# Kernel optimization log

Measured on AMD Instinct MI355X. Metric: run time of the kernel, lower is better.

The kernel has to match this reference:

```python
import jax, jax.numpy as jnp
import numpy as np
from jax import lax

N, C, RC, H, W = 2, 256, 32, 64, 64  # RC = C // 8


def conv1x1(x, w, b):
    # x: [n,c,h,w], w: [o,c], b: [o]
    return jnp.einsum('nchw,oc->nohw', x, w) + b[None, :, None, None]


def conv3x3(x, w, b):
    # x: [n,c,h,w], w: [o,i,3,3]
    y = lax.conv_general_dilated(x, w, window_strides=(1, 1), padding='SAME',
                                 dimension_numbers=('NCHW', 'OIHW', 'NCHW'))
    return y + b[None, :, None, None]


def setup_inputs() -> dict:
    key = jax.random.key(0)
    ks = jax.random.split(key, 16)
    p = lambda k, s: jax.random.normal(k, s, dtype=jnp.float32) * 0.02
    z = lambda o: jnp.zeros((o,), jnp.float32)
    return {
        'rgb_feat': jax.random.normal(ks[0], (N, C, H, W), jnp.float32),
        'chm_feat': jax.random.normal(ks[1], (N, C, H, W), jnp.float32),
        'rgb_q_w': p(ks[2], (RC, C)), 'rgb_q_b': z(RC),
        'rgb_k_w': p(ks[3], (RC, C)), 'rgb_k_b': z(RC),
        'rgb_v_w': p(ks[4], (C, C)), 'rgb_v_b': z(C),
        'depth_q_w': p(ks[5], (RC, C)), 'depth_q_b': z(RC),
        'depth_k_w': p(ks[6], (RC, C)), 'depth_k_b': z(RC),
        'depth_v_w': p(ks[7], (C, C)), 'depth_v_b': z(C),
        'gate_w': p(ks[8], (C, 2 * C)), 'gate_b': z(C),
        'fus1_w': p(ks[9], (2 * C, 2 * C)), 'fus1_b': z(2 * C),
        'fus2_w': p(ks[10], (2 * C, 2 * C, 3, 3)), 'fus2_b': z(2 * C),
        'fus3_w': p(ks[11], (C, 2 * C)), 'fus3_b': z(C),
        'skip_w': p(ks[12], (C, 2 * C)), 'skip_b': z(C),
    }


def reference(rgb_feat, chm_feat,
              rgb_q_w, rgb_q_b, rgb_k_w, rgb_k_b, rgb_v_w, rgb_v_b,
              depth_q_w, depth_q_b, depth_k_w, depth_k_b, depth_v_w, depth_v_b,
              gate_w, gate_b, fus1_w, fus1_b, fus2_w, fus2_b,
              fus3_w, fus3_b, skip_w, skip_b):
    n, c, h, w = rgb_feat.shape
    hw = h * w
    flat = lambda t: t.reshape(n, t.shape[1], hw)

    rq = flat(conv1x1(rgb_feat, rgb_q_w, rgb_q_b))       # [n,rc,hw]
    rk = flat(conv1x1(rgb_feat, rgb_k_w, rgb_k_b))       # [n,rc,hw]
    rv = flat(conv1x1(rgb_feat, rgb_v_w, rgb_v_b))       # [n,c,hw]
    dq = flat(conv1x1(chm_feat, depth_q_w, depth_q_b))   # [n,rc,hw]
    dk = flat(conv1x1(chm_feat, depth_k_w, depth_k_b))   # [n,rc,hw]
    dv = flat(conv1x1(chm_feat, depth_v_w, depth_v_b))   # [n,c,hw]

    # rgb branch attended with depth-derived attention
    rgb_attn = jax.nn.softmax(jnp.einsum('nri,nrj->nij', dq, dk), axis=-1)  # [n,hw,hw]
    br = jnp.einsum('nci,nij->ncj', rv, rgb_attn).reshape(rgb_feat.shape) + rgb_feat

    # depth branch attended with rgb-derived attention
    depth_attn = jax.nn.softmax(jnp.einsum('nri,nrj->nij', rq, rk), axis=-1)
    bd = jnp.einsum('nci,nij->ncj', dv, depth_attn).reshape(chm_feat.shape) + chm_feat

    cat = jnp.concatenate([br, bd], axis=1)              # [n,2c,h,w]
    g = jax.nn.sigmoid(conv1x1(cat, gate_w, gate_b))     # [n,c,h,w]
    c_fused = br * g + bd * (1.0 - g)
    d_fused = br * bd
    f = jnp.concatenate([c_fused, d_fused], axis=1)      # [n,2c,h,w]

    y = jax.nn.relu(conv1x1(f, fus1_w, fus1_b))
    y = jax.nn.relu(conv3x3(y, fus2_w, fus2_b))
    y = conv1x1(y, fus3_w, fus3_b)
    fused = y + conv1x1(f, skip_w, skip_b)
    return fused
```

## Files before the change

kernel.cpp:

```cpp
#include <hip/hip_runtime.h>
#include <stdint.h>


typedef __bf16 bf16_t;
typedef __bf16 bf16x8 __attribute__((ext_vector_type(8)));
typedef float f32x4 __attribute__((ext_vector_type(4)));

#define HW 4096
#define NB 2

__device__ inline f32x4 mfma_bf16(bf16x8 a, bf16x8 b, f32x4 c) {
    return __builtin_amdgcn_mfma_f32_16x16x32_bf16(a, b, c, 0, 0, 0);
}

#define LBAR()                                                                 \
    do {                                                                       \
        asm volatile("s_waitcnt lgkmcnt(0)" ::: "memory");                     \
        __builtin_amdgcn_s_barrier();                                          \
        __builtin_amdgcn_sched_barrier(0);                                     \
    } while (0)

#define MAXJOB 12
struct CvtJobs {
    const float* src[MAXJOB];
    bf16_t* dst[MAXJOB];
    int vend[MAXJOB];
    int rowlen[MAXJOB];
    int rowstride[MAXJOB];
    int rowoff[MAXJOB];
};

__global__ __launch_bounds__(256) void prep_k(CvtJobs J, int totalvec, int cvtBlocks,
                                              const float* __restrict__ fus2_src,
                                              bf16_t* __restrict__ fus2_dst,
                                              const float* qr, const float* kr,
                                              const float* qd, const float* kd,
                                              const float* sb, const float* fb,
                                              float* BQK_R, float* BQK_D, float* BSUM) {
    const int b = blockIdx.x, t = threadIdx.x;
    if (b < cvtBlocks) {
        int gv = b * 256 + t;
        if (gv >= totalvec) return;
        int j = 0;
        while (gv >= J.vend[j]) j++;
        int vbase = (j == 0) ? 0 : J.vend[j - 1];
        int e = (gv - vbase) * 8;
        const float* s = J.src[j] + e;
        float4 f0 = *(const float4*)s;
        float4 f1 = *(const float4*)(s + 4);
        bf16x8 o;
        o[0] = (bf16_t)f0.x; o[1] = (bf16_t)f0.y; o[2] = (bf16_t)f0.z; o[3] = (bf16_t)f0.w;
        o[4] = (bf16_t)f1.x; o[5] = (bf16_t)f1.y; o[6] = (bf16_t)f1.z; o[7] = (bf16_t)f1.w;
        int di = e;
        if (J.rowlen[j])
            di = (e / J.rowlen[j]) * J.rowstride[j] + J.rowoff[j] + (e % J.rowlen[j]);
        *(bf16x8*)(J.dst[j] + di) = o;
    } else if (b < cvtBlocks + 9216) {
        int idx = (b - cvtBlocks) * 256 + t;
        int o = idx / 4608;
        int tt = idx % 4608;
        int t9 = tt / 512;
        int c  = tt % 512;
        fus2_dst[idx] = (bf16_t)fus2_src[(size_t)o * 4608 + c * 9 + t9];
    } else {
        if (t < 32) {
            BQK_R[t] = qr[t]; BQK_R[32 + t] = kr[t];
            BQK_D[t] = qd[t]; BQK_D[32 + t] = kd[t];
        }
        BSUM[t] = sb[t] + fb[t];
    }
}

__global__ __launch_bounds__(512) void proj_k(const bf16_t* __restrict__ WV_R,
                                              const bf16_t* __restrict__ WV_D,
                                              const bf16_t* __restrict__ WQK_R,
                                              const bf16_t* __restrict__ WQK_D,
                                              const bf16_t* __restrict__ XB,
                                              const float* __restrict__ vb_r,
                                              const float* __restrict__ vb_d,
                                              const float* __restrict__ bqk_r,
                                              const float* __restrict__ bqk_d,
                                              bf16_t* __restrict__ V4,
                                              bf16_t* __restrict__ QKT) {
    __shared__ bf16_t Bt[2][64][72];
    const int t = threadIdx.x, b = blockIdx.x;
    const int w = t >> 6, lane = t & 63, quad = lane >> 4, l16 = lane & 15;

    f32x4 zero = {0.f, 0.f, 0.f, 0.f};
    f32x4 acc[4] = {zero, zero, zero, zero};

    if (b < 512) {
        const int mb = b & 1, jb = (b >> 1) & 63, n = b >> 7;
        const bf16_t* Au = (n >= 2) ? WV_D : WV_R;
        const float* biasu = (n >= 2) ? vb_d : vb_r;
        const bf16_t* Bb = XB + (size_t)n * (256 * HW) + jb * 64;
        const bf16_t* Arow = Au + (size_t)(mb * 128 + w * 16 + l16) * 256 + quad * 8;

        bf16x8 v0 = *(const bf16x8*)(Bb + (size_t)lane * HW + w * 8);
        for (int k0 = 0; k0 < 256; k0 += 64) {
            LBAR();
#pragma unroll
            for (int e = 0; e < 8; e++) Bt[0][w * 8 + e][lane] = v0[e];
            LBAR();
            const int kn = (k0 + 64 < 256) ? k0 + 64 : 0;
            bf16x8 vp = *(const bf16x8*)(Bb + (size_t)(kn + lane) * HW + w * 8);
            bf16x8 a0 = *(const bf16x8*)(Arow + k0);
            bf16x8 a1 = *(const bf16x8*)(Arow + k0 + 32);
#pragma unroll
            for (int ns = 0; ns < 4; ns++) {
                bf16x8 b0 = *(const bf16x8*)&Bt[0][ns * 16 + l16][quad * 8];
                bf16x8 b1 = *(const bf16x8*)&Bt[0][ns * 16 + l16][32 + quad * 8];
                acc[ns] = mfma_bf16(a0, b0, acc[ns]);
                acc[ns] = mfma_bf16(a1, b1, acc[ns]);
            }
            v0 = vp;
        }
#pragma unroll
        for (int ns = 0; ns < 4; ns++) {
#pragma unroll
            for (int rr = 0; rr < 4; rr++) {
                int m = mb * 128 + w * 16 + quad * 4 + rr;
                int col = jb * 64 + ns * 16 + l16;
                V4[(size_t)n * 256 * HW + (size_t)m * HW + col] =
                    (bf16_t)(acc[ns][rr] + biasu[m]);
            }
        }
    } else {
        const int qb = b - 512;
        const int n2 = qb >> 5, jpair = qb & 31;
        const int g = w >> 2, wg = w & 3;
        const int jb = jpair * 2 + g;
        const bf16_t* Au = (n2 >= 2) ? WQK_D : WQK_R;
        const float* biasu = (n2 >= 2) ? bqk_d : bqk_r;
        const bf16_t* Bb = XB + (size_t)n2 * (256 * HW) + jb * 64;
        const bf16_t* Arow = Au + (size_t)(wg * 16 + l16) * 256 + quad * 8;

        bf16x8 v0 = *(const bf16x8*)(Bb + (size_t)lane * HW + wg * 16);
        bf16x8 v1 = *(const bf16x8*)(Bb + (size_t)lane * HW + wg * 16 + 8);
        for (int k0 = 0; k0 < 256; k0 += 64) {
            LBAR();
#pragma unroll
            for (int e = 0; e < 8; e++) Bt[g][wg * 16 + e][lane] = v0[e];
#pragma unroll
            for (int e = 0; e < 8; e++) Bt[g][wg * 16 + 8 + e][lane] = v1[e];
            LBAR();
            const int kn = (k0 + 64 < 256) ? k0 + 64 : 0;
            bf16x8 p0 = *(const bf16x8*)(Bb + (size_t)(kn + lane) * HW + wg * 16);
            bf16x8 p1 = *(const bf16x8*)(Bb + (size_t)(kn + lane) * HW + wg * 16 + 8);
            bf16x8 a0 = *(const bf16x8*)(Arow + k0);
            bf16x8 a1 = *(const bf16x8*)(Arow + k0 + 32);
#pragma unroll
            for (int ns = 0; ns < 4; ns++) {
                bf16x8 b0 = *(const bf16x8*)&Bt[g][ns * 16 + l16][quad * 8];
                bf16x8 b1 = *(const bf16x8*)&Bt[g][ns * 16 + l16][32 + quad * 8];
                acc[ns] = mfma_bf16(a0, b0, acc[ns]);
                acc[ns] = mfma_bf16(a1, b1, acc[ns]);
            }
            v0 = p0; v1 = p1;
        }
        const float scl = (wg < 2) ? 1.44269504f : 1.0f;
#pragma unroll
        for (int ns = 0; ns < 4; ns++) {
            int col = jb * 64 + ns * 16 + l16;
            union { bf16_t h[4]; unsigned long long u; } pk;
#pragma unroll
            for (int rr = 0; rr < 4; rr++) {
                int m = wg * 16 + quad * 4 + rr;
                pk.h[rr] = (bf16_t)((acc[ns][rr] + biasu[m]) * scl);
            }
            *(unsigned long long*)(QKT +
                ((size_t)n2 * HW + col) * 64 + wg * 16 + quad * 4) = pk.u;
        }
    }
}

template <int EPI, bool OUT_BF16>
__global__ __launch_bounds__(512) void gemm_k(const bf16_t* __restrict__ A,
                                              const bf16_t* __restrict__ A2,
                                              const bf16_t* __restrict__ B,
                                              const float* __restrict__ bias,
                                              const float* __restrict__ bias2,
                                              void* __restrict__ outp,
                                              const void* __restrict__ aux,
                                              int M, int K, size_t strideB, size_t strideO) {
    __shared__ bf16_t Bt[64][72];
    const int t = threadIdx.x;
    const int mb = blockIdx.x, jb = blockIdx.y, n = blockIdx.z;
    const int w = t >> 6, lane = t & 63, quad = lane >> 4, l16 = lane & 15;

    const bf16_t* Au = (n >= 2) ? A2 : A;
    const float* biasu = (n >= 2) ? bias2 : bias;

    const bf16_t* Bb = B + (size_t)n * strideB + jb * 64;

    f32x4 zero = {0.f, 0.f, 0.f, 0.f};
    f32x4 acc[4] = {zero, zero, zero, zero};

    const bf16_t* Arow = Au + (size_t)(mb * 128 + w * 16 + l16) * K + quad * 8;

    bf16x8 v0 = *(const bf16x8*)(Bb + (size_t)lane * HW + w * 8);
    for (int k0 = 0; k0 < K; k0 += 64) {
        LBAR();
#pragma unroll
        for (int e = 0; e < 8; e++) Bt[w * 8 + e][lane] = v0[e];
        LBAR();
        const int kn = (k0 + 64 < K) ? k0 + 64 : 0;
        bf16x8 vp = *(const bf16x8*)(Bb + (size_t)(kn + lane) * HW + w * 8);
        bf16x8 a0 = *(const bf16x8*)(Arow + k0);
        bf16x8 a1 = *(const bf16x8*)(Arow + k0 + 32);
#pragma unroll
        for (int ns = 0; ns < 4; ns++) {
            bf16x8 b0 = *(const bf16x8*)&Bt[ns * 16 + l16][quad * 8];
            bf16x8 b1 = *(const bf16x8*)&Bt[ns * 16 + l16][32 + quad * 8];
            acc[ns] = mfma_bf16(a0, b0, acc[ns]);
            acc[ns] = mfma_bf16(a1, b1, acc[ns]);
        }
        v0 = vp;
    }

    if (EPI == 7) {
        const int m_base = mb * 128 + w * 16 + quad * 4;
#pragma unroll
        for (int ns = 0; ns < 4; ns++) {
            int col = jb * 64 + ns * 16 + l16;
            union { bf16_t h[4]; unsigned long long u; } pk;
#pragma unroll
            for (int rr = 0; rr < 4; rr++) {
                float v = acc[ns][rr] + biasu[m_base + rr];
                pk.h[rr] = (bf16_t)(v > 0.f ? v : 0.f);
            }
            *(unsigned long long*)((bf16_t*)outp +
                ((size_t)n * HW + col) * 512 + m_base) = pk.u;
        }
    } else if (EPI == 5) {
        const bf16_t* catp = (const bf16_t*)aux;
        bf16_t* f = (bf16_t*)outp;
#pragma unroll
        for (int ns = 0; ns < 4; ns++) {
#pragma unroll
            for (int rr = 0; rr < 4; rr++) {
                int m = mb * 128 + w * 16 + quad * 4 + rr;
                int col = jb * 64 + ns * 16 + l16;
                float v = acc[ns][rr] + biasu[m];
                float g = 1.f / (1.f + __expf(-v));
                size_t base = (size_t)n * 512 * HW + (size_t)m * HW + col;
                float br = (float)catp[base];
                float bd = (float)catp[base + (size_t)256 * HW];
                size_t ob = (size_t)n * 1024 * HW + (size_t)m * HW + col;
                f[ob] = (bf16_t)(br * g + bd * (1.f - g));
                f[ob + (size_t)256 * HW] = (bf16_t)(br * bd);
            }
        }
    } else {
#pragma unroll
        for (int ns = 0; ns < 4; ns++) {
#pragma unroll
            for (int rr = 0; rr < 4; rr++) {
                int m = mb * 128 + w * 16 + quad * 4 + rr;
                int col = jb * 64 + ns * 16 + l16;
                float v = acc[ns][rr] + biasu[m];
                size_t oi = (size_t)n * strideO + (size_t)m * HW + col;
                if (OUT_BF16) ((bf16_t*)outp)[oi] = (bf16_t)v;
                else ((float*)outp)[oi] = v;
            }
        }
    }
}

__global__ __launch_bounds__(256) void conv3_k(const bf16_t* __restrict__ A,
                                               const bf16_t* __restrict__ Y1n,
                                               const float* __restrict__ bias,
                                               bf16_t* __restrict__ outp,
                                               size_t strideN) {
    __shared__ bf16_t kTn[198][72];
    const int t = threadIdx.x;
    const int lin = blockIdx.x;
    const int n = lin & 1, mb = (lin >> 1) & 3, y = lin >> 3;
    const int w = t >> 6, lane = t & 63, quad = lane >> 4, l16 = lane & 15;

    f32x4 zero = {0.f, 0.f, 0.f, 0.f};
    f32x4 acc[2][4];
#pragma unroll
    for (int i = 0; i < 2; i++)
#pragma unroll
        for (int j = 0; j < 4; j++) acc[i][j] = zero;

    const bf16_t* Yb = Y1n + (size_t)n * HW * 512;

    const bf16_t* Arow0 = A + (size_t)(mb * 128 + w * 32 + l16) * 4608 + quad * 8;
    const bf16_t* Arow1 = Arow0 + (size_t)16 * 4608;

    int pxs[7], seg[7], gidx[7];
    bool ok[7], act[7];
#pragma unroll
    for (int i = 0; i < 7; i++) {
        int slot = t + i * 256;
        act[i] = slot < 1584;
        int ps = act[i] ? (slot >> 3) : 0;
        pxs[i] = ps;
        seg[i] = slot & 7;
        int r = ps / 66, xm = ps % 66;
        int yy = y + r - 1, xx = xm - 1;
        ok[i] = act[i] && ((unsigned)yy < 64u) && ((unsigned)xx < 64u);
        gidx[i] = ok[i] ? (yy * 64 + xx) : 0;
    }

    bf16x8 vals[7];
#pragma unroll
    for (int i = 0; i < 7; i++) {
        bf16x8 v;
        if (ok[i]) {
            v = *(const bf16x8*)(Yb + (size_t)gidx[i] * 512 + seg[i] * 8);
        } else {
#pragma unroll
            for (int e = 0; e < 8; e++) v[e] = (bf16_t)0.f;
        }
        vals[i] = v;
    }

    for (int c0 = 0; c0 < 512; c0 += 64) {
        LBAR();
#pragma unroll
        for (int i = 0; i < 7; i++)
            if (act[i]) *(bf16x8*)&kTn[pxs[i]][seg[i] * 8] = vals[i];
        LBAR();

        const int cn = (c0 + 64) & 511;
#pragma unroll
        for (int i = 0; i < 7; i++) {
            bf16x8 v;
            if (ok[i]) {
                v = *(const bf16x8*)(Yb + (size_t)gidx[i] * 512 + cn + seg[i] * 8);
            } else {
#pragma unroll
                for (int e = 0; e < 8; e++) v[e] = (bf16_t)0.f;
            }
            vals[i] = v;
        }

#pragma unroll
        for (int t9 = 0; t9 < 9; t9++) {
            const int dy = t9 / 3, dx = t9 % 3;
            const bf16_t* ap0 = Arow0 + t9 * 512 + c0;
            const bf16_t* ap1 = Arow1 + t9 * 512 + c0;
            bf16x8 a00 = *(const bf16x8*)(ap0);
            bf16x8 a01 = *(const bf16x8*)(ap0 + 32);
            bf16x8 a10 = *(const bf16x8*)(ap1);
            bf16x8 a11 = *(const bf16x8*)(ap1 + 32);
#pragma unroll
            for (int ns = 0; ns < 4; ns++) {
                int p = dy * 66 + ns * 16 + l16 + dx;
                bf16x8 b0 = *(const bf16x8*)&kTn[p][quad * 8];
                bf16x8 b1 = *(const bf16x8*)&kTn[p][32 + quad * 8];
                acc[0][ns] = mfma_bf16(a00, b0, acc[0][ns]);
                acc[0][ns] = mfma_bf16(a01, b1, acc[0][ns]);
                acc[1][ns] = mfma_bf16(a10, b0, acc[1][ns]);
                acc[1][ns] = mfma_bf16(a11, b1, acc[1][ns]);
            }
        }
    }

#pragma unroll
    for (int ms = 0; ms < 2; ms++) {
#pragma unroll
        for (int ns = 0; ns < 4; ns++) {
#pragma unroll
            for (int rr = 0; rr < 4; rr++) {
                int m = mb * 128 + w * 32 + ms * 16 + quad * 4 + rr;
                int x = ns * 16 + l16;
                float v = acc[ms][ns][rr] + bias[m];
                v = v > 0.f ? v : 0.f;
                outp[(size_t)n * strideN + (size_t)m * HW + y * 64 + x] = (bf16_t)v;
            }
        }
    }
}

#define PSTEP(P, ASC, ASN, ITN)                                                \
    {                                                                          \
        _Pragma("unroll")                                                      \
        for (int ns = 0; ns < 4; ns++) {                                       \
            f32x4 s = mfma_bf16(ASC, bS[ns], zero);                            \
            union { bf16_t h[4]; unsigned long long u; } pk;                   \
            float zs = 0.f;                                                    \
            _Pragma("unroll")                                                  \
            for (int rr = 0; rr < 4; rr++) {                                   \
                pk.h[rr] = (bf16_t)__builtin_amdgcn_exp2f(s[rr]);              \
                zs += (float)pk.h[rr];                                         \
            }                                                                  \
            zacc[ns] += zs;                                                    \
            *(unsigned long long*)&PT[P][ns * 16 + l16][w * 16 + quad * 4] = pk.u; \
        }                                                                      \
        ASN = *(const bf16x8*)(Qa + (size_t)((ITN) & 63) * (64 * 64));         \
        asm volatile("s_waitcnt lgkmcnt(0)" ::: "memory");                     \
        __builtin_amdgcn_s_barrier();                                          \
        __builtin_amdgcn_sched_barrier(0);                                     \
    }

#define CSTEP(P, AVC, AVN, ITN)                                                \
    {                                                                          \
        __builtin_amdgcn_s_barrier();                                          \
        __builtin_amdgcn_sched_barrier(0);                                     \
        __builtin_amdgcn_s_setprio(1);                                         \
        _Pragma("unroll")                                                      \
        for (int ns = 0; ns < 4; ns++) {                                       \
            bf16x8 b0 = *(const bf16x8*)&PT[P][ns * 16 + l16][quad * 8];       \
            bf16x8 b1 = *(const bf16x8*)&PT[P][ns * 16 + l16][32 + quad * 8];  \
            _Pragma("unroll")                                                  \
            for (int ct = 0; ct < 4; ct++) {                                   \
                acc[ct][ns] = mfma_bf16(AVC[ct][0], b0, acc[ct][ns]);          \
                acc[ct][ns] = mfma_bf16(AVC[ct][1], b1, acc[ct][ns]);          \
            }                                                                  \
        }                                                                      \
        __builtin_amdgcn_s_setprio(0);                                         \
        _Pragma("unroll")                                                      \
        for (int ct = 0; ct < 4; ct++) {                                       \
            AVN[ct][0] = *(const bf16x8*)(Vr[ct] + ((ITN) & 63) * 64);         \
            AVN[ct][1] = *(const bf16x8*)(Vr[ct] + ((ITN) & 63) * 64 + 32);    \
        }                                                                      \
        asm volatile("s_waitcnt lgkmcnt(0)" ::: "memory");                     \
        __builtin_amdgcn_sched_barrier(0);                                     \
    }

__global__ __launch_bounds__(512) void attn3_k(const bf16_t* __restrict__ QKT,
                                               const bf16_t* __restrict__ V,
                                               const float* __restrict__ rgb_feat,
                                               const float* __restrict__ chm_feat,
                                               bf16_t* __restrict__ CAT) {
    __shared__ bf16_t PT[2][64][72];
    __shared__ float Zp[4][64];
    const int t = threadIdx.x;
    const int lin = blockIdx.x;
    const int z = (lin >> 1) & 3;
    const int jb = ((lin >> 3) << 1) | (lin & 1);
    const int w = t >> 6, lane = t & 63, quad = lane >> 4, l16 = lane & 15;
    const int qs = z ^ 2, n = z & 1;

    const bf16_t* Q = QKT + (size_t)qs * HW * 64;
    f32x4 zero = {0.f, 0.f, 0.f, 0.f};

    if (w < 4) {
        bf16x8 bS[4];
#pragma unroll
        for (int ns = 0; ns < 4; ns++)
            bS[ns] = *(const bf16x8*)(Q + (size_t)(jb * 64 + ns * 16 + l16) * 64 + 32 + quad * 8);
        float zacc[4] = {0.f, 0.f, 0.f, 0.f};
        const bf16_t* Qa = Q + (size_t)(w * 16 + l16) * 64 + quad * 8;

        bf16x8 aSa, aSb;
        aSa = *(const bf16x8*)Qa;

        for (int ii = 0; ii < 32; ii++) {
            PSTEP(0, aSa, aSb, 2 * ii + 1);
            PSTEP(1, aSb, aSa, 2 * ii + 2);
        }

#pragma unroll
        for (int ns = 0; ns < 4; ns++) {
            zacc[ns] += __shfl_xor(zacc[ns], 16, 64);
            zacc[ns] += __shfl_xor(zacc[ns], 32, 64);
        }
        if (lane < 16) {
#pragma unroll
            for (int ns = 0; ns < 4; ns++) Zp[w][ns * 16 + lane] = zacc[ns];
        }
        __syncthreads();
    } else {
        const int wc = w - 4;
        f32x4 acc[4][4];
#pragma unroll
        for (int i = 0; i < 4; i++)
#pragma unroll
            for (int j = 0; j < 4; j++) acc[i][j] = zero;

        const bf16_t* Vr[4];
#pragma unroll
        for (int ct = 0; ct < 4; ct++)
            Vr[ct] = V + ((size_t)z * 256 + wc * 64 + ct * 16 + l16) * HW + quad * 8;

        bf16x8 aVa[4][2], aVb[4][2];
#pragma unroll
        for (int ct = 0; ct < 4; ct++) {
            aVa[ct][0] = *(const bf16x8*)(Vr[ct]);
            aVa[ct][1] = *(const bf16x8*)(Vr[ct] + 32);
        }

        for (int ii = 0; ii < 32; ii++) {
            CSTEP(0, aVa, aVb, 2 * ii + 1);
            CSTEP(1, aVb, aVa, 2 * ii + 2);
        }

        __syncthreads();

        float rz[4];
#pragma unroll
        for (int ns = 0; ns < 4; ns++) {
            float ssum = 0.f;
#pragma unroll
            for (int ww = 0; ww < 4; ww++) ssum += Zp[ww][ns * 16 + l16];
            rz[ns] = 1.f / ssum;
        }

        const float* feat = ((z < 2) ? rgb_feat : chm_feat) + (size_t)n * 256 * HW;
        bf16_t* outp = CAT + (size_t)n * 512 * HW + (size_t)(z < 2 ? 0 : 256) * HW;
#pragma unroll
        for (int ct = 0; ct < 4; ct++) {
#pragma unroll
            for (int ns = 0; ns < 4; ns++) {
#pragma unroll
                for (int rr = 0; rr < 4; rr++) {
                    int c = wc * 64 + ct * 16 + quad * 4 + rr;
                    int col = jb * 64 + ns * 16 + l16;
                    float v = acc[ct][ns][rr] * rz[ns] + feat[(size_t)c * HW + col];
                    outp[(size_t)c * HW + col] = (bf16_t)v;
                }
            }
        }
    }
}

extern "C" void kernel_launch(void* const* d_in, const int* in_sizes, int n_in,
                              void* d_out, int out_size, void* d_ws, size_t ws_size,
                              hipStream_t stream) {
    (void)in_sizes; (void)n_in; (void)out_size; (void)ws_size;

    const float* rgb_feat  = (const float*)d_in[0];
    const float* chm_feat  = (const float*)d_in[1];
    const float* rgb_q_w   = (const float*)d_in[2];
    const float* rgb_q_b   = (const float*)d_in[3];
    const float* rgb_k_w   = (const float*)d_in[4];
    const float* rgb_k_b   = (const float*)d_in[5];
    const float* rgb_v_w   = (const float*)d_in[6];
    const float* rgb_v_b   = (const float*)d_in[7];
    const float* depth_q_w = (const float*)d_in[8];
    const float* depth_q_b = (const float*)d_in[9];
    const float* depth_k_w = (const float*)d_in[10];
    const float* depth_k_b = (const float*)d_in[11];
    const float* depth_v_w = (const float*)d_in[12];
    const float* depth_v_b = (const float*)d_in[13];
    const float* gate_w    = (const float*)d_in[14];
    const float* gate_b    = (const float*)d_in[15];
    const float* fus1_w    = (const float*)d_in[16];
    const float* fus1_b    = (const float*)d_in[17];
    const float* fus2_w    = (const float*)d_in[18];
    const float* fus2_b    = (const float*)d_in[19];
    const float* fus3_w    = (const float*)d_in[20];
    const float* fus3_b    = (const float*)d_in[21];
    const float* skip_w    = (const float*)d_in[22];
    const float* skip_b    = (const float*)d_in[23];

    char* ws = (char*)d_ws;
    size_t off = 0;
    auto alloc = [&](size_t bytes) -> char* {
        char* p = ws + off;
        off += (bytes + 255) & ~(size_t)255;
        return p;
    };

    bf16_t* WQK_R = (bf16_t*)alloc(64 * 256 * 2);
    bf16_t* WQK_D = (bf16_t*)alloc(64 * 256 * 2);
    bf16_t* WV_R  = (bf16_t*)alloc(256 * 256 * 2);
    bf16_t* WV_D  = (bf16_t*)alloc(256 * 256 * 2);
    bf16_t* WGATE = (bf16_t*)alloc(256 * 512 * 2);
    bf16_t* WFUS1 = (bf16_t*)alloc(512 * 512 * 2);
    bf16_t* WFUS2 = (bf16_t*)alloc(512 * 4608 * 2);
    bf16_t* WCAT  = (bf16_t*)alloc(256 * 1024 * 2);
    float*  BQK_R = (float*)alloc(64 * 4);
    float*  BQK_D = (float*)alloc(64 * 4);
    float*  BSUM  = (float*)alloc(256 * 4);
    bf16_t* XB    = (bf16_t*)alloc((size_t)4 * 256 * HW * 2);
    bf16_t* QKT   = (bf16_t*)alloc((size_t)4 * HW * 64 * 2);
    bf16_t* V4    = (bf16_t*)alloc((size_t)4 * 256 * HW * 2);
    bf16_t* CAT   = (bf16_t*)alloc((size_t)NB * 512 * HW * 2);
    bf16_t* FY    = (bf16_t*)alloc((size_t)NB * 1024 * HW * 2);
    bf16_t* Y1    = (bf16_t*)alloc((size_t)NB * HW * 512 * 2);

    bf16_t* XR = XB;
    bf16_t* XC = XB + (size_t)2 * 256 * HW;

    CvtJobs J;
    int cum = 0, nj = 0;
    auto addjob = [&](const float* s, bf16_t* d, int cnt, int rl, int rs, int ro) {
        J.src[nj] = s; J.dst[nj] = d; cum += cnt / 8; J.vend[nj] = cum;
        J.rowlen[nj] = rl; J.rowstride[nj] = rs; J.rowoff[nj] = ro; nj++;
    };
    addjob(rgb_feat, XR, NB * 256 * HW, 0, 0, 0);
    addjob(chm_feat, XC, NB * 256 * HW, 0, 0, 0);
    addjob(rgb_q_w, WQK_R, 32 * 256, 0, 0, 0);
    addjob(rgb_k_w, WQK_R + 32 * 256, 32 * 256, 0, 0, 0);
    addjob(depth_q_w, WQK_D, 32 * 256, 0, 0, 0);
    addjob(depth_k_w, WQK_D + 32 * 256, 32 * 256, 0, 0, 0);
    addjob(rgb_v_w, WV_R, 256 * 256, 0, 0, 0);
    addjob(depth_v_w, WV_D, 256 * 256, 0, 0, 0);
    addjob(gate_w, WGATE, 256 * 512, 0, 0, 0);
    addjob(fus1_w, WFUS1, 512 * 512, 0, 0, 0);
    addjob(skip_w, WCAT, 256 * 512, 512, 1024, 0);
    addjob(fus3_w, WCAT, 256 * 512, 512, 1024, 512);
    int totalvec = cum;
    int cvtBlocks = (totalvec + 255) / 256;
    int prepBlocks = cvtBlocks + 9216 + 1;
    prep_k<<<dim3(prepBlocks), 256, 0, stream>>>(
        J, totalvec, cvtBlocks, fus2_w, WFUS2,
        rgb_q_b, rgb_k_b, depth_q_b, depth_k_b, skip_b, fus3_b,
        BQK_R, BQK_D, BSUM);

    proj_k<<<dim3(640), 512, 0, stream>>>(
        WV_R, WV_D, WQK_R, WQK_D, XB, rgb_v_b, depth_v_b, BQK_R, BQK_D, V4, QKT);

    attn3_k<<<dim3(256), 512, 0, stream>>>(QKT, V4, rgb_feat, chm_feat, CAT);

    gemm_k<5, true><<<dim3(2, 64, NB), 512, 0, stream>>>(
        WGATE, WGATE, CAT, gate_b, gate_b, FY, CAT, 256, 512, (size_t)512 * HW, 0);

    gemm_k<7, true><<<dim3(4, 64, NB), 512, 0, stream>>>(
        WFUS1, WFUS1, FY, fus1_b, fus1_b, Y1, nullptr, 512, 512, (size_t)1024 * HW, 0);

    conv3_k<<<dim3(512), 256, 0, stream>>>(WFUS2, Y1, fus2_b,
                                           FY + (size_t)512 * HW, (size_t)1024 * HW);

    gemm_k<0, false><<<dim3(2, 64, NB), 512, 0, stream>>>(
        WCAT, WCAT, FY, BSUM, BSUM, d_out, nullptr, 256, 1024, (size_t)1024 * HW, (size_t)256 * HW);
}
```

Baseline: 328.6 us.

## Widen conv3x3 tile to 256 output channels, prefetch weights, repad LDS rows

The 3x3 conv kernel now computes 256 output channels per block instead of 128, with four 16-row A fragments per wave. This halves the grid and reuses each staged LDS input tile across twice as many output rows. Weight fragments for the next tap are loaded into registers while the current tap's MFMAs run, to hide global-load latency. LDS row padding changes from 72 to 74 bf16 in all kernels to alter bank mapping. Risks: 148-byte rows break the 16-byte alignment that the bf16x8 LDS reads assume, register pressure rises sharply, and 256 blocks of 4 waves may leave the GPU under-occupied.

```diff
diff --git a/kernel.cpp b/kernel.cpp
--- a/kernel.cpp
+++ b/kernel.cpp
@@ -82,7 +82,7 @@
                                               const float* __restrict__ bqk_d,
                                               bf16_t* __restrict__ V4,
                                               bf16_t* __restrict__ QKT) {
-    __shared__ bf16_t Bt[2][64][72];
+    __shared__ bf16_t Bt[2][64][74];
     const int t = threadIdx.x, b = blockIdx.x;
     const int w = t >> 6, lane = t & 63, quad = lane >> 4, l16 = lane & 15;
 
@@ -183,7 +183,7 @@
                                               void* __restrict__ outp,
                                               const void* __restrict__ aux,
                                               int M, int K, size_t strideB, size_t strideO) {
-    __shared__ bf16_t Bt[64][72];
+    __shared__ bf16_t Bt[64][74];
     const int t = threadIdx.x;
     const int mb = blockIdx.x, jb = blockIdx.y, n = blockIdx.z;
     const int w = t >> 6, lane = t & 63, quad = lane >> 4, l16 = lane & 15;
@@ -272,23 +272,25 @@
                                                const float* __restrict__ bias,
                                                bf16_t* __restrict__ outp,
                                                size_t strideN) {
-    __shared__ bf16_t kTn[198][72];
+    __shared__ bf16_t kTn[198][74];
     const int t = threadIdx.x;
     const int lin = blockIdx.x;
-    const int n = lin & 1, mb = (lin >> 1) & 3, y = lin >> 3;
+    const int n = lin & 1, mb = (lin >> 1) & 1, y = lin >> 2;
     const int w = t >> 6, lane = t & 63, quad = lane >> 4, l16 = lane & 15;
 
     f32x4 zero = {0.f, 0.f, 0.f, 0.f};
-    f32x4 acc[2][4];
-#pragma unroll
-    for (int i = 0; i < 2; i++)
+    f32x4 acc[4][4];
+#pragma unroll
+    for (int i = 0; i < 4; i++)
 #pragma unroll
         for (int j = 0; j < 4; j++) acc[i][j] = zero;
 
     const bf16_t* Yb = Y1n + (size_t)n * HW * 512;
 
-    const bf16_t* Arow0 = A + (size_t)(mb * 128 + w * 32 + l16) * 4608 + quad * 8;
-    const bf16_t* Arow1 = Arow0 + (size_t)16 * 4608;
+    const bf16_t* Arow[4];
+#pragma unroll
+    for (int h = 0; h < 4; h++)
+        Arow[h] = A + (size_t)(mb * 256 + w * 64 + h * 16 + l16) * 4608 + quad * 8;
 
     int pxs[7], seg[7], gidx[7];
     bool ok[7], act[7];
@@ -318,6 +320,13 @@
         vals[i] = v;
     }
 
+    bf16x8 aC[4][2], aN[4][2];
+#pragma unroll
+    for (int h = 0; h < 4; h++) {
+        aC[h][0] = *(const bf16x8*)(Arow[h]);
+        aC[h][1] = *(const bf16x8*)(Arow[h] + 32);
+    }
+
     for (int c0 = 0; c0 < 512; c0 += 64) {
         LBAR();
 #pragma unroll
@@ -341,34 +350,41 @@
 #pragma unroll
         for (int t9 = 0; t9 < 9; t9++) {
             const int dy = t9 / 3, dx = t9 % 3;
-            const bf16_t* ap0 = Arow0 + t9 * 512 + c0;
-            const bf16_t* ap1 = Arow1 + t9 * 512 + c0;
-            bf16x8 a00 = *(const bf16x8*)(ap0);
-            bf16x8 a01 = *(const bf16x8*)(ap0 + 32);
-            bf16x8 a10 = *(const bf16x8*)(ap1);
-            bf16x8 a11 = *(const bf16x8*)(ap1 + 32);
+            const int nc = (t9 == 8) ? cn : c0;
+            const int nt = (t9 == 8) ? 0 : t9 + 1;
+#pragma unroll
+            for (int h = 0; h < 4; h++) {
+                aN[h][0] = *(const bf16x8*)(Arow[h] + nt * 512 + nc);
+                aN[h][1] = *(const bf16x8*)(Arow[h] + nt * 512 + nc + 32);
+            }
 #pragma unroll
             for (int ns = 0; ns < 4; ns++) {
                 int p = dy * 66 + ns * 16 + l16 + dx;
                 bf16x8 b0 = *(const bf16x8*)&kTn[p][quad * 8];
                 bf16x8 b1 = *(const bf16x8*)&kTn[p][32 + quad * 8];
-                acc[0][ns] = mfma_bf16(a00, b0, acc[0][ns]);
-                acc[0][ns] = mfma_bf16(a01, b1, acc[0][ns]);
-                acc[1][ns] = mfma_bf16(a10, b0, acc[1][ns]);
-                acc[1][ns] = mfma_bf16(a11, b1, acc[1][ns]);
-            }
-        }
-    }
-
-#pragma unroll
-    for (int ms = 0; ms < 2; ms++) {
+#pragma unroll
+                for (int h = 0; h < 4; h++) {
+                    acc[h][ns] = mfma_bf16(aC[h][0], b0, acc[h][ns]);
+                    acc[h][ns] = mfma_bf16(aC[h][1], b1, acc[h][ns]);
+                }
+            }
+#pragma unroll
+            for (int h = 0; h < 4; h++) {
+                aC[h][0] = aN[h][0];
+                aC[h][1] = aN[h][1];
+            }
+        }
+    }
+
+#pragma unroll
+    for (int h = 0; h < 4; h++) {
 #pragma unroll
         for (int ns = 0; ns < 4; ns++) {
 #pragma unroll
             for (int rr = 0; rr < 4; rr++) {
-                int m = mb * 128 + w * 32 + ms * 16 + quad * 4 + rr;
+                int m = mb * 256 + w * 64 + h * 16 + quad * 4 + rr;
                 int x = ns * 16 + l16;
-                float v = acc[ms][ns][rr] + bias[m];
+                float v = acc[h][ns][rr] + bias[m];
                 v = v > 0.f ? v : 0.f;
                 outp[(size_t)n * strideN + (size_t)m * HW + y * 64 + x] = (bf16_t)v;
             }
@@ -427,7 +443,7 @@
                                                const float* __restrict__ rgb_feat,
                                                const float* __restrict__ chm_feat,
                                                bf16_t* __restrict__ CAT) {
-    __shared__ bf16_t PT[2][64][72];
+    __shared__ bf16_t PT[2][64][74];
     __shared__ float Zp[4][64];
     const int t = threadIdx.x;
     const int lin = blockIdx.x;
@@ -615,7 +631,7 @@
     gemm_k<7, true><<<dim3(4, 64, NB), 512, 0, stream>>>(
         WFUS1, WFUS1, FY, fus1_b, fus1_b, Y1, nullptr, 512, 512, (size_t)1024 * HW, 0);
 
-    conv3_k<<<dim3(512), 256, 0, stream>>>(WFUS2, Y1, fus2_b,
+    conv3_k<<<dim3(256), 256, 0, stream>>>(WFUS2, Y1, fus2_b,
                                            FY + (size_t)512 * HW, (size_t)1024 * HW);
 
     gemm_k<0, false><<<dim3(2, 64, NB), 512, 0, stream>>>(
```

After: 350.3 us. +6.6%, slower.
